# Performance work log

Hardware: AMD Instinct MI355X
Metric: run time of the kernel (lower is better)

Reference implementation:

```python
import jax, jax.numpy as jnp
import numpy as np

B, TT, C, H, T = 4, 4096, 1024, 16, 128
K = C // H  # head size (rk and v head sizes equal here)
HEAD_DIV = 8.0  # head_size_divisor
EPS = 1e-5  # GroupNorm eps
LAYER_ID, N_LAYER = 12, 24


def setup_inputs() -> dict:
    key = jax.random.key(0)
    ks = jax.random.split(key, 8)
    r01 = LAYER_ID / (N_LAYER - 1)
    r1a0 = 1.0 - LAYER_ID / N_LAYER
    ddd = (jnp.arange(C, dtype=jnp.float32) / C).reshape(1, 1, C)
    h = jnp.arange(H, dtype=jnp.float32)
    scale = 0.02
    return {
        "xq": jax.random.normal(ks[0], (B, TT, C), jnp.float32),
        "time_mix_k": ddd ** r1a0,
        "time_mix_v": ddd ** r1a0 + 0.3 * r01,
        "time_mix_r": ddd ** (0.5 * r1a0),
        "time_mix_g": ddd ** (0.5 * r1a0),
        "time_decay": -8.0 + 7.0 * (h / (H - 1)) ** (0.7 + 1.3 * r01),
        "time_faaaa": r01 * (1.0 - h / (H - 1)),
        "W_r": jax.random.normal(ks[1], (C, C), jnp.float32) * scale,
        "W_k": jax.random.normal(ks[2], (C, C), jnp.float32) * scale,
        "W_v": jax.random.normal(ks[3], (C, C), jnp.float32) * scale,
        "W_g": jax.random.normal(ks[4], (C, C), jnp.float32) * scale,
        "W_o": jax.random.normal(ks[5], (C, C), jnp.float32) * scale,
        "ln_w": jnp.ones((C,), jnp.float32),
        "ln_b": jnp.zeros((C,), jnp.float32),
    }


def reference(xq, time_mix_k, time_mix_v, time_mix_r, time_mix_g,
              time_decay, time_faaaa, W_r, W_k, W_v, W_g, W_o, ln_w, ln_b):
    x = xq
    B_, TT_, C_ = x.shape
    N = TT_ // T  # number of chunks
    # time shift: xx[:, t] = x[:, t-1], xx[:, 0] = 0
    xx = jnp.pad(x, ((0, 0), (1, 0), (0, 0)))[:, :-1]
    xr = x * time_mix_r + xx * (1 - time_mix_r)
    xk = x * time_mix_k + xx * (1 - time_mix_k)
    xv = x * time_mix_v + xx * (1 - time_mix_v)
    xg = x * time_mix_g + xx * (1 - time_mix_g)
    r = (xr @ W_r.T).reshape(B_, TT_, H, K).transpose(0, 2, 1, 3)  # (B,H,TT,K)
    k = (xk @ W_k.T).reshape(B_, TT_, H, K).transpose(0, 2, 1, 3)
    v = (xv @ W_v.T).reshape(B_, TT_, H, K).transpose(0, 2, 1, 3)
    g = jax.nn.silu(xg @ W_g.T)  # (B,TT,C)

    decay = jnp.exp(-jnp.exp(time_decay))  # (H,)
    u = time_faaaa  # (H,)
    ws = decay ** T  # per-chunk state decay (H,)
    i_idx = jnp.arange(T)
    wb = decay[:, None] ** i_idx                # (H,T): decay^i
    wk = decay[:, None] ** (T - 1 - i_idx)      # (H,T): decay^(T-1-j)
    diff = i_idx[:, None] - i_idx[None, :]      # i - j
    pw = decay[:, None, None] ** jnp.maximum(diff - 1, 0)
    # lower-triangular intra-chunk decay: decay^(i-j-1) for i>j, u on diag
    w_mat = jnp.where(diff > 0, pw, 0.0) + jnp.eye(T, dtype=x.dtype) * u[:, None, None]  # (H,T,T)

    # chunked layout: (N, B, H, T, K)
    rc = r.reshape(B_, H, N, T, K).transpose(2, 0, 1, 3, 4)
    kc = k.reshape(B_, H, N, T, K).transpose(2, 0, 1, 3, 4)
    vc = v.reshape(B_, H, N, T, K).transpose(2, 0, 1, 3, 4)
    s0 = jnp.zeros((B_, H, K, K), x.dtype)

    def step(s, chunk):
        rr, kk, vv = chunk
        att = jnp.einsum('bhik,bhjk->bhij', rr, kk) * w_mat
        out = att @ vv + jnp.einsum('bhik,bhkv->bhiv', rr, s) * wb[None, :, :, None]
        s_new = ws[None, :, None, None] * s + jnp.einsum(
            'bhjk,bhjv->bhkv', kk * wk[None, :, :, None], vv)
        return s_new, out

    _, xo = jax.lax.scan(step, s0, (rc, kc, vc))  # xo: (N,B,H,T,K)
    xo = xo.transpose(1, 0, 3, 2, 4).reshape(B_, TT_, H, K)

    # GroupNorm(H groups) over channels, applied to x / head_size_divisor
    y = xo / HEAD_DIV
    mu = y.mean(-1, keepdims=True)
    var = y.var(-1, keepdims=True)
    y = (y - mu) / jnp.sqrt(var + EPS)
    y = y * ln_w.reshape(H, K) + ln_b.reshape(H, K)
    y = y.reshape(B_, TT_, C_)
    return (y * g) @ W_o.T
```

## Files before the change

### kernel.cpp

```cpp
#include <hip/hip_runtime.h>
#include <hip/hip_bf16.h>
#include <stdint.h>

#define C_DIM 1024
#define H_DIM 16
#define K_DIM 64
#define T_CH 128
#define TT_DIM 4096
#define B_DIM 4
#define N_CH 32
#define M_ROWS 16384

typedef __attribute__((ext_vector_type(8))) __bf16 bf16x8;
typedef __attribute__((ext_vector_type(4))) float floatx4;

__device__ __forceinline__ float bf2f(ushort u) {
  union { uint32_t i; float f; } v; v.i = ((uint32_t)u) << 16; return v.f;
}
__device__ __forceinline__ ushort f2bf(float f) {
  union { float f; uint32_t i; } v; v.f = f;
  return (ushort)((v.i + 0x7fffu + ((v.i >> 16) & 1u)) >> 16);
}

#define GLOAD_LDS16(g, l)                                                     \
  __builtin_amdgcn_global_load_lds(                                           \
      (const __attribute__((address_space(1))) void*)(g),                     \
      (__attribute__((address_space(3))) void*)(l), 16, 0, 0)

__global__ __launch_bounds__(256) void mix_kernel(
    const float* __restrict__ x,
    const float* __restrict__ mk, const float* __restrict__ mv,
    const float* __restrict__ mr, const float* __restrict__ mg,
    ushort* __restrict__ xr, ushort* __restrict__ xk,
    ushort* __restrict__ xv, ushort* __restrict__ xg) {
  long idx = (long)blockIdx.x * 256 + threadIdx.x;
  long e = idx * 4;
  int c = (int)(e & (C_DIM - 1));
  long row = e >> 10;
  int t = (int)(row & (TT_DIM - 1));
  floatx4 xc = *(const floatx4*)(x + e);
  floatx4 xp = {0.f, 0.f, 0.f, 0.f};
  if (t != 0) xp = *(const floatx4*)(x + e - C_DIM);
  floatx4 d = xc - xp;
  floatx4 vk = *(const floatx4*)(mk + c);
  floatx4 vv = *(const floatx4*)(mv + c);
  floatx4 vr = *(const floatx4*)(mr + c);
  floatx4 vg = *(const floatx4*)(mg + c);
  floatx4 ok = xp + d * vk;
  floatx4 ov = xp + d * vv;
  floatx4 orr = xp + d * vr;
  floatx4 og = xp + d * vg;
  union { ushort u[4]; uint2 q; } pk;
#define ST(dst, val)                                                          \
  pk.u[0] = f2bf(val.x); pk.u[1] = f2bf(val.y);                               \
  pk.u[2] = f2bf(val.z); pk.u[3] = f2bf(val.w);                               \
  *(uint2*)((dst) + e) = pk.q;
  ST(xk, ok) ST(xv, ov) ST(xr, orr) ST(xg, og)
#undef ST
}

__global__ __launch_bounds__(256) void wconv_kernel(
    const float* __restrict__ w0, const float* __restrict__ w1,
    const float* __restrict__ w2, const float* __restrict__ w3,
    const float* __restrict__ w4, ushort* __restrict__ o) {
  long idx = (long)blockIdx.x * 256 + threadIdx.x;
  long e = idx * 4;
  int wi = (int)(e >> 20);
  long off = e & ((1L << 20) - 1);
  const float* src = wi == 0 ? w0 : wi == 1 ? w1 : wi == 2 ? w2 : wi == 3 ? w3 : w4;
  floatx4 vv = *(const floatx4*)(src + off);
  union { ushort u[4]; uint2 q; } pk;
  pk.u[0] = f2bf(vv.x); pk.u[1] = f2bf(vv.y);
  pk.u[2] = f2bf(vv.z); pk.u[3] = f2bf(vv.w);
  *(uint2*)(o + e) = pk.q;
}

#define BARX() __builtin_amdgcn_s_barrier()
#define SCHEDB() __builtin_amdgcn_sched_barrier(0)
#define VMW4() asm volatile("s_waitcnt vmcnt(4)" ::: "memory")
#define VMW0() asm volatile("s_waitcnt vmcnt(0)" ::: "memory")
#define LGKW() asm volatile("s_waitcnt lgkmcnt(0)" ::: "memory")

template <int EPI>
__global__ __launch_bounds__(512, 2) void gemm_bt(
    const ushort* __restrict__ A, const ushort* __restrict__ Bt,
    void* __restrict__ Cout) {
  __shared__ __align__(16) ushort smem[65536];
  const int tid = threadIdx.x;
  const int lane = tid & 63, w = tid >> 6;
  const int q = lane >> 4, l16 = lane & 15;
  const int wm = w >> 2, wn = w & 3;
  const int id = blockIdx.x;
  const int wg = (id & 7) * 32 + (id >> 3);
  const int bm = wg >> 2, bn = wg & 3;

  const int r8 = tid >> 3;
  const int c8 = ((tid & 7) ^ (r8 & 7)) * 8;
  const ushort* gA = A + (long)(bm * 256 + r8) * C_DIM + c8;
  const ushort* gB = Bt + (long)(bn * 256 + r8) * C_DIM + c8;

  const char* sB = (const char*)smem;
  const int arow = (wm * 128 + l16) * 128;
  const int brow = (wn * 64 + l16) * 128;
  const int swz = (l16 & 7) << 4;
  const int csv[2] = {(q << 4) ^ swz, ((4 + q) << 4) ^ swz};

  floatx4 acc[8][4] = {};
  bf16x8 af[4][2];
  bf16x8 bfv[4][2];

#define STAGE(ISA, sl, hh, tile)                                              \
  do {                                                                        \
    const ushort* g_ = (ISA ? gA : gB) + ((hh) * 131072 + (tile) * 64);       \
    ushort* l_ = smem + ((ISA ? 0 : 32768) + (sl) * 16384 + (hh) * 8192 +     \
                         w * 512);                                            \
    GLOAD_LDS16(g_, l_);                                                      \
    GLOAD_LDS16(g_ + 65536, l_ + 4096);                                       \
  } while (0)

#define READ_A(sl, qr)                                                        \
  do {                                                                        \
    _Pragma("unroll") for (int i_ = 0; i_ < 4; ++i_) {                        \
      af[i_][0] = *(const bf16x8*)(sB + (sl) * 32768 + arow + (qr) * 8192 +   \
                                   i_ * 2048 + csv[0]);                       \
      af[i_][1] = *(const bf16x8*)(sB + (sl) * 32768 + arow + (qr) * 8192 +   \
                                   i_ * 2048 + csv[1]);                       \
    }                                                                         \
  } while (0)

#define READ_B(sl, qc)                                                        \
  do {                                                                        \
    _Pragma("unroll") for (int j_ = 0; j_ < 2; ++j_) {                        \
      bfv[(qc) * 2 + j_][0] = *(const bf16x8*)(sB + 65536 + (sl) * 32768 +    \
                                               brow + (qc) * 4096 +           \
                                               j_ * 2048 + csv[0]);           \
      bfv[(qc) * 2 + j_][1] = *(const bf16x8*)(sB + 65536 + (sl) * 32768 +    \
                                               brow + (qc) * 4096 +           \
                                               j_ * 2048 + csv[1]);           \
    }                                                                         \
  } while (0)

#define MFMA_Q(qr, qc)                                                        \
  do {                                                                        \
    __builtin_amdgcn_s_setprio(1);                                            \
    _Pragma("unroll") for (int i_ = 0; i_ < 4; ++i_)                          \
        _Pragma("unroll") for (int j_ = 0; j_ < 2; ++j_) {                    \
      acc[(qr) * 4 + i_][(qc) * 2 + j_] =                                     \
          __builtin_amdgcn_mfma_f32_16x16x32_bf16(                            \
              af[i_][0], bfv[(qc) * 2 + j_][0],                               \
              acc[(qr) * 4 + i_][(qc) * 2 + j_], 0, 0, 0);                    \
      acc[(qr) * 4 + i_][(qc) * 2 + j_] =                                     \
          __builtin_amdgcn_mfma_f32_16x16x32_bf16(                            \
              af[i_][1], bfv[(qc) * 2 + j_][1],                               \
              acc[(qr) * 4 + i_][(qc) * 2 + j_], 0, 0, 0);                    \
    }                                                                         \
    __builtin_amdgcn_s_setprio(0);                                            \
  } while (0)

  STAGE(1, 0, 0, 0); STAGE(1, 0, 1, 0);
  STAGE(0, 0, 0, 0); STAGE(0, 0, 1, 0);
  STAGE(0, 1, 0, 1); STAGE(0, 1, 1, 1);
  VMW4();
  BARX();
  SCHEDB();
  READ_B(0, 0);

#pragma unroll 1
  for (int i = 0; i < 7; ++i) {
    const int t1 = 2 * i + 1, tn0 = 2 * i + 2, tn1 = 2 * i + 3;
    READ_A(0, 0); STAGE(1, 1, 0, t1);
    BARX(); SCHEDB(); READ_B(0, 1); MFMA_Q(0, 0); LGKW(); BARX();
    STAGE(1, 1, 1, t1);
    BARX(); SCHEDB(); MFMA_Q(0, 1); LGKW(); BARX();
    READ_A(0, 1); STAGE(0, 0, 0, tn0);
    BARX(); SCHEDB(); MFMA_Q(1, 0); LGKW(); BARX();
    STAGE(0, 0, 1, tn0); VMW4();
    BARX(); SCHEDB(); READ_B(1, 0); MFMA_Q(1, 1); LGKW(); BARX();
    READ_A(1, 0); STAGE(1, 0, 0, tn0);
    BARX(); SCHEDB(); READ_B(1, 1); MFMA_Q(0, 0); LGKW(); BARX();
    STAGE(1, 0, 1, tn0);
    BARX(); SCHEDB(); MFMA_Q(0, 1); LGKW(); BARX();
    READ_A(1, 1); STAGE(0, 1, 0, tn1);
    BARX(); SCHEDB(); MFMA_Q(1, 0); LGKW(); BARX();
    STAGE(0, 1, 1, tn1); VMW4();
    BARX(); SCHEDB(); READ_B(0, 0); MFMA_Q(1, 1); LGKW(); BARX();
  }
  READ_A(0, 0); STAGE(1, 1, 0, 15);
  BARX(); SCHEDB(); READ_B(0, 1); MFMA_Q(0, 0); LGKW(); BARX();
  STAGE(1, 1, 1, 15);
  BARX(); SCHEDB(); MFMA_Q(0, 1); LGKW(); BARX();
  READ_A(0, 1);
  BARX(); SCHEDB(); MFMA_Q(1, 0); LGKW(); BARX();
  VMW0();
  BARX(); SCHEDB(); READ_B(1, 0); MFMA_Q(1, 1); LGKW(); BARX();
  READ_A(1, 0);
  BARX(); SCHEDB(); READ_B(1, 1); MFMA_Q(0, 0); LGKW(); BARX();
  BARX(); SCHEDB(); MFMA_Q(0, 1); LGKW(); BARX();
  READ_A(1, 1);
  BARX(); SCHEDB(); MFMA_Q(1, 0); LGKW(); BARX();
  BARX(); MFMA_Q(1, 1);

  const int row0 = bm * 256 + wm * 128 + q * 4;
  const int col0 = bn * 256 + wn * 64 + l16;
#pragma unroll
  for (int fi = 0; fi < 8; ++fi)
#pragma unroll
    for (int fj = 0; fj < 4; ++fj)
#pragma unroll
      for (int rg = 0; rg < 4; ++rg) {
        long off = (long)(row0 + fi * 16 + rg) * C_DIM + col0 + fj * 16;
        float val = acc[fi][fj][rg];
        if (EPI == 1) val = val / (1.f + expf(-val));
        if (EPI == 2)
          ((float*)Cout)[off] = val;
        else
          ((ushort*)Cout)[off] = f2bf(val);
      }
#undef STAGE
#undef READ_A
#undef READ_B
#undef MFMA_Q
}

__global__ __launch_bounds__(256) void chunk_state(
    const ushort* __restrict__ kB, const ushort* __restrict__ vB,
    const float* __restrict__ td, ushort* __restrict__ Zc) {
  __shared__ __align__(16) ushort vt_s[64 * 136];
  __shared__ __align__(16) ushort kwt_s[64 * 136];
  int blk = blockIdx.x;
  int bh = blk >> 5, n = blk & 31;
  int b = bh >> 4, h = bh & 15;
  int tid = threadIdx.x;
  int lane = tid & 63, w = tid >> 6;
  int q = lane >> 4, l16 = lane & 15;
  float etd = expf(td[h]);
  long cbase = ((long)b * TT_DIM + n * T_CH) * C_DIM + h * K_DIM;

#pragma unroll
  for (int it = 0; it < 4; it++) {
    int chunk = it * 256 + tid;
    int row = chunk >> 3;
    int cc = (chunk & 7) * 8;
    long ga = cbase + (long)row * C_DIM + cc;
    uint4 kv4 = *(const uint4*)(kB + ga);
    uint4 vv4 = *(const uint4*)(vB + ga);
    float wkj = expf(-(float)(T_CH - 1 - row) * etd);
    const ushort* kp = (const ushort*)&kv4;
    const ushort* vp = (const ushort*)&vv4;
    int cb2 = row >> 3;
#pragma unroll
    for (int e2 = 0; e2 < 8; e2++) {
      int vr = cc + e2;
      int ph = vr * 136 + ((cb2 ^ ((vr >> 3) & 7)) << 3) + (row & 7);
      kwt_s[ph] = f2bf(bf2f(kp[e2]) * wkj);
      vt_s[ph] = vp[e2];
    }
  }
  __syncthreads();

  floatx4 accZ[4] = {};
#pragma unroll
  for (int js = 0; js < 128; js += 32) {
    int cb = q + (js >> 3);
    int vrA = w * 16 + l16;
    bf16x8 av = *(const bf16x8*)&vt_s[vrA * 136 + ((cb ^ ((vrA >> 3) & 7)) << 3)];
    bf16x8 bk3[4];
#pragma unroll
    for (int kt = 0; kt < 4; kt++) {
      int vrB = kt * 16 + l16;
      bk3[kt] = *(const bf16x8*)&kwt_s[vrB * 136 + ((cb ^ ((vrB >> 3) & 7)) << 3)];
    }
#pragma unroll
    for (int kt = 0; kt < 4; kt++)
      accZ[kt] = __builtin_amdgcn_mfma_f32_16x16x32_bf16(av, bk3[kt], accZ[kt], 0, 0, 0);
  }
  long zbase = (long)blk * 4096;
#pragma unroll
  for (int kt = 0; kt < 4; kt++)
#pragma unroll
    for (int rg = 0; rg < 4; rg++)
      Zc[zbase + (w * 16 + q * 4 + rg) * 64 + kt * 16 + l16] = f2bf(accZ[kt][rg]);
}

__global__ __launch_bounds__(256) void state_scan(
    const ushort* __restrict__ Zc, const float* __restrict__ td,
    ushort* __restrict__ Sb) {
  long tg = (long)blockIdx.x * 256 + threadIdx.x;
  int bh = (int)(tg >> 12);
  int e = (int)(tg & 4095);
  int h = bh & 15;
  float wsf = expf(-128.f * expf(td[h]));
  float s = 0.f;
  long base = (long)bh * N_CH * 4096 + e;
#pragma unroll
  for (int n = 0; n < N_CH; n++) {
    Sb[base + n * 4096] = f2bf(s);
    s = wsf * s + bf2f(Zc[base + n * 4096]);
  }
}

__global__ __launch_bounds__(512, 4) void chunk_out(
    const ushort* __restrict__ rB, const ushort* __restrict__ kB,
    const ushort* __restrict__ vB, const ushort* __restrict__ gBuf,
    const ushort* __restrict__ Sb,
    const float* __restrict__ td, const float* __restrict__ tf,
    const float* __restrict__ lnw, const float* __restrict__ lnb,
    ushort* __restrict__ gy) {
  __shared__ __align__(16) ushort rr_s[128 * 72];
  __shared__ __align__(16) ushort un_s[128 * 136];
  __shared__ __align__(16) ushort vt_s[64 * 136];
  __shared__ __align__(16) ushort z_s[64 * 72];
  __shared__ float pw_s[128];

  int blk = blockIdx.x;
  int bh = blk >> 5, n = blk & 31;
  int b = bh >> 4, h = bh & 15;
  int tid = threadIdx.x;
  int lane = tid & 63, w = tid >> 6;
  int q = lane >> 4, l16 = lane & 15;

  float etd = expf(td[h]);
  float u = tf[h];
  long cbase = ((long)b * TT_DIM + n * T_CH) * C_DIM + h * K_DIM;

  if (tid < 128) pw_s[tid] = expf(-(float)tid * etd);

#pragma unroll
  for (int it = 0; it < 2; it++) {
    int chunk = it * 512 + tid;
    int row = chunk >> 3;
    int cc = (chunk & 7) * 8;
    long ga = cbase + (long)row * C_DIM + cc;
    *(uint4*)&rr_s[row * 72 + cc] = *(const uint4*)(rB + ga);
    *(uint4*)&un_s[row * 136 + cc] = *(const uint4*)(kB + ga);
    uint4 vv4 = *(const uint4*)(vB + ga);
    const ushort* vp = (const ushort*)&vv4;
    int cb2 = row >> 3;
#pragma unroll
    for (int e2 = 0; e2 < 8; e2++) {
      int vr = cc + e2;
      vt_s[vr * 136 + ((cb2 ^ ((vr >> 3) & 7)) << 3) + (row & 7)] = vp[e2];
    }
  }
  {
    long sbase = (long)blk * 4096;
    int v = tid >> 3, c0 = (tid & 7) * 8;
    *(uint4*)&z_s[v * 72 + c0] = *(const uint4*)(Sb + sbase + v * 64 + c0);
  }
  __syncthreads();

  int ar0 = (w >> 1) * 32, ac0 = (w & 1) * 64;
  floatx4 accA[2][4] = {};
#pragma unroll
  for (int ks = 0; ks < 64; ks += 32) {
    bf16x8 af[2], bk2[4];
#pragma unroll
    for (int i = 0; i < 2; i++)
      af[i] = *(const bf16x8*)&rr_s[(ar0 + i * 16 + l16) * 72 + q * 8 + ks];
#pragma unroll
    for (int j = 0; j < 4; j++)
      bk2[j] = *(const bf16x8*)&un_s[(ac0 + j * 16 + l16) * 136 + q * 8 + ks];
#pragma unroll
    for (int mi = 0; mi < 2; mi++)
#pragma unroll
      for (int nj = 0; nj < 4; nj++)
        accA[mi][nj] = __builtin_amdgcn_mfma_f32_16x16x32_bf16(
            af[mi], bk2[nj], accA[mi][nj], 0, 0, 0);
  }

  int i0 = w * 16;
  floatx4 accB[4] = {};
#pragma unroll
  for (int ks = 0; ks < 64; ks += 32) {
    bf16x8 af2 = *(const bf16x8*)&rr_s[(i0 + l16) * 72 + q * 8 + ks];
    bf16x8 bz[4];
#pragma unroll
    for (int vt2 = 0; vt2 < 4; vt2++)
      bz[vt2] = *(const bf16x8*)&z_s[(vt2 * 16 + l16) * 72 + q * 8 + ks];
#pragma unroll
    for (int vt2 = 0; vt2 < 4; vt2++)
      accB[vt2] = __builtin_amdgcn_mfma_f32_16x16x32_bf16(
          af2, bz[vt2], accB[vt2], 0, 0, 0);
  }
  __syncthreads();

#pragma unroll
  for (int mi = 0; mi < 2; mi++)
#pragma unroll
    for (int nj = 0; nj < 4; nj++)
#pragma unroll
      for (int rg = 0; rg < 4; rg++) {
        int i = ar0 + mi * 16 + q * 4 + rg;
        int j = ac0 + nj * 16 + l16;
        float wv = 0.f;
        if (i > j) wv = pw_s[i - j - 1];
        else if (i == j) wv = u;
        un_s[i * 136 + j] = f2bf(accA[mi][nj][rg] * wv);
      }
  __syncthreads();

  floatx4 accO[4] = {};
#pragma unroll
  for (int js = 0; js < 128; js += 32) {
    bf16x8 af3 = *(const bf16x8*)&un_s[(i0 + l16) * 136 + q * 8 + js];
    int cb = q + (js >> 3);
    bf16x8 bv[4];
#pragma unroll
    for (int vt2 = 0; vt2 < 4; vt2++) {
      int vr = vt2 * 16 + l16;
      bv[vt2] = *(const bf16x8*)&vt_s[vr * 136 + ((cb ^ ((vr >> 3) & 7)) << 3)];
    }
#pragma unroll
    for (int vt2 = 0; vt2 < 4; vt2++)
      accO[vt2] = __builtin_amdgcn_mfma_f32_16x16x32_bf16(
          af3, bv[vt2], accO[vt2], 0, 0, 0);
  }

#pragma unroll
  for (int rg = 0; rg < 4; rg++) {
    int i = i0 + q * 4 + rg;
    float wbi = pw_s[i];
    float vals[4];
    float s1 = 0.f, s2 = 0.f;
#pragma unroll
    for (int vt2 = 0; vt2 < 4; vt2++) {
      float val = accO[vt2][rg] + wbi * accB[vt2][rg];
      vals[vt2] = val; s1 += val; s2 += val * val;
    }
#pragma unroll
    for (int mm = 1; mm < 16; mm <<= 1) {
      s1 += __shfl_xor(s1, mm, 64);
      s2 += __shfl_xor(s2, mm, 64);
    }
    float mu = s1 * (1.f / 64.f);
    float va = s2 * (1.f / 64.f) - mu * mu;
    float rinv = rsqrtf(va + 64.f * 1e-5f);
    long rowg = (long)b * TT_DIM + n * T_CH + i;
#pragma unroll
    for (int vt2 = 0; vt2 < 4; vt2++) {
      int c = h * K_DIM + vt2 * 16 + l16;
      float y = (vals[vt2] - mu) * rinv * lnw[c] + lnb[c];
      float gf = bf2f(gBuf[rowg * C_DIM + c]);
      gy[rowg * C_DIM + c] = f2bf(y * gf);
    }
  }
}

extern "C" void kernel_launch(void* const* d_in, const int* in_sizes, int n_in,
                              void* d_out, int out_size, void* d_ws,
                              size_t ws_size, hipStream_t stream) {
  const float* xq  = (const float*)d_in[0];
  const float* tmk = (const float*)d_in[1];
  const float* tmv = (const float*)d_in[2];
  const float* tmr = (const float*)d_in[3];
  const float* tmg = (const float*)d_in[4];
  const float* td  = (const float*)d_in[5];
  const float* tf  = (const float*)d_in[6];
  const float* Wr  = (const float*)d_in[7];
  const float* Wk  = (const float*)d_in[8];
  const float* Wv  = (const float*)d_in[9];
  const float* Wg  = (const float*)d_in[10];
  const float* Wo  = (const float*)d_in[11];
  const float* lnw = (const float*)d_in[12];
  const float* lnb = (const float*)d_in[13];

  char* ws = (char*)d_ws;
  const size_t BUF = (size_t)M_ROWS * C_DIM * 2;
  ushort* b0 = (ushort*)(ws + 0 * BUF);
  ushort* b1 = (ushort*)(ws + 1 * BUF);
  ushort* b2 = (ushort*)(ws + 2 * BUF);
  ushort* b3 = (ushort*)(ws + 3 * BUF);
  ushort* wcv = (ushort*)(ws + 4 * BUF);
  const ushort* wr_b = wcv;
  const ushort* wk_b = wcv + (1 << 20);
  const ushort* wv_b = wcv + 2 * (1 << 20);
  const ushort* wg_b = wcv + 3 * (1 << 20);
  const ushort* wo_b = wcv + 4 * (1 << 20);
  ushort* Zc = (ushort*)(ws + 4 * BUF + 5 * (2 << 20));
  ushort* Sb = Zc + (size_t)64 * N_CH * 4096;
  ushort* rbuf = (ushort*)d_out;

  mix_kernel<<<16384, 256, 0, stream>>>(xq, tmk, tmv, tmr, tmg, b0, b1, b2, b3);
  wconv_kernel<<<5120, 256, 0, stream>>>(Wr, Wk, Wv, Wg, Wo, wcv);

  gemm_bt<0><<<256, 512, 0, stream>>>(b0, wr_b, rbuf);
  gemm_bt<0><<<256, 512, 0, stream>>>(b1, wk_b, b0);
  gemm_bt<0><<<256, 512, 0, stream>>>(b2, wv_b, b1);
  gemm_bt<1><<<256, 512, 0, stream>>>(b3, wg_b, b2);

  chunk_state<<<2048, 256, 0, stream>>>(b0, b1, td, Zc);
  state_scan<<<1024, 256, 0, stream>>>(Zc, td, Sb);
  chunk_out<<<2048, 512, 0, stream>>>(rbuf, b0, b1, b2, Sb, td, tf, lnw, lnb, b3);

  gemm_bt<2><<<256, 512, 0, stream>>>(b3, wo_b, (float*)d_out);
}
```

Before: 407.3 us.

## Pair projection GEMMs into shared launches and widen elementwise kernels to 8 elements

Combines the four input projection GEMMs into two launches of 512 workgroups each, so every launch fills the GPU with two independent GEMMs rather than 256 workgroups at a time. Buffers are reassigned so r and k land in the two halves of the fp32 output buffer, which serves as scratch. The mix and weight-conversion kernels now handle 8 elements per thread with 16-byte stores, halving their grid sizes. The aim is less launch overhead and better CU occupancy during the projections. This relies on the output buffer being large enough to hold two bf16 activation tensors before the final GEMM overwrites it.

```diff
diff --git a/kernel.cpp b/kernel.cpp
--- a/kernel.cpp
+++ b/kernel.cpp
@@ -34,28 +34,34 @@
     ushort* __restrict__ xr, ushort* __restrict__ xk,
     ushort* __restrict__ xv, ushort* __restrict__ xg) {
   long idx = (long)blockIdx.x * 256 + threadIdx.x;
-  long e = idx * 4;
+  long e = idx * 8;
   int c = (int)(e & (C_DIM - 1));
   long row = e >> 10;
   int t = (int)(row & (TT_DIM - 1));
-  floatx4 xc = *(const floatx4*)(x + e);
-  floatx4 xp = {0.f, 0.f, 0.f, 0.f};
-  if (t != 0) xp = *(const floatx4*)(x + e - C_DIM);
-  floatx4 d = xc - xp;
-  floatx4 vk = *(const floatx4*)(mk + c);
-  floatx4 vv = *(const floatx4*)(mv + c);
-  floatx4 vr = *(const floatx4*)(mr + c);
-  floatx4 vg = *(const floatx4*)(mg + c);
-  floatx4 ok = xp + d * vk;
-  floatx4 ov = xp + d * vv;
-  floatx4 orr = xp + d * vr;
-  floatx4 og = xp + d * vg;
-  union { ushort u[4]; uint2 q; } pk;
-#define ST(dst, val)                                                          \
-  pk.u[0] = f2bf(val.x); pk.u[1] = f2bf(val.y);                               \
-  pk.u[2] = f2bf(val.z); pk.u[3] = f2bf(val.w);                               \
-  *(uint2*)((dst) + e) = pk.q;
-  ST(xk, ok) ST(xv, ov) ST(xr, orr) ST(xg, og)
+  floatx4 xc0 = *(const floatx4*)(x + e);
+  floatx4 xc1 = *(const floatx4*)(x + e + 4);
+  floatx4 xp0 = {0.f, 0.f, 0.f, 0.f};
+  floatx4 xp1 = {0.f, 0.f, 0.f, 0.f};
+  if (t != 0) {
+    xp0 = *(const floatx4*)(x + e - C_DIM);
+    xp1 = *(const floatx4*)(x + e - C_DIM + 4);
+  }
+  floatx4 d0 = xc0 - xp0;
+  floatx4 d1 = xc1 - xp1;
+  union { ushort u[8]; uint4 q; } pk;
+#define ST(dst, mptr)                                                         \
+  {                                                                           \
+    floatx4 m0 = *(const floatx4*)((mptr) + c);                               \
+    floatx4 m1 = *(const floatx4*)((mptr) + c + 4);                           \
+    floatx4 o0 = xp0 + d0 * m0;                                               \
+    floatx4 o1 = xp1 + d1 * m1;                                               \
+    pk.u[0] = f2bf(o0.x); pk.u[1] = f2bf(o0.y);                               \
+    pk.u[2] = f2bf(o0.z); pk.u[3] = f2bf(o0.w);                               \
+    pk.u[4] = f2bf(o1.x); pk.u[5] = f2bf(o1.y);                               \
+    pk.u[6] = f2bf(o1.z); pk.u[7] = f2bf(o1.w);                               \
+    *(uint4*)((dst) + e) = pk.q;                                              \
+  }
+  ST(xk, mk) ST(xv, mv) ST(xr, mr) ST(xg, mg)
 #undef ST
 }
 
@@ -64,15 +70,18 @@
     const float* __restrict__ w2, const float* __restrict__ w3,
     const float* __restrict__ w4, ushort* __restrict__ o) {
   long idx = (long)blockIdx.x * 256 + threadIdx.x;
-  long e = idx * 4;
+  long e = idx * 8;
   int wi = (int)(e >> 20);
   long off = e & ((1L << 20) - 1);
   const float* src = wi == 0 ? w0 : wi == 1 ? w1 : wi == 2 ? w2 : wi == 3 ? w3 : w4;
-  floatx4 vv = *(const floatx4*)(src + off);
-  union { ushort u[4]; uint2 q; } pk;
-  pk.u[0] = f2bf(vv.x); pk.u[1] = f2bf(vv.y);
-  pk.u[2] = f2bf(vv.z); pk.u[3] = f2bf(vv.w);
-  *(uint2*)(o + e) = pk.q;
+  floatx4 v0 = *(const floatx4*)(src + off);
+  floatx4 v1 = *(const floatx4*)(src + off + 4);
+  union { ushort u[8]; uint4 q; } pk;
+  pk.u[0] = f2bf(v0.x); pk.u[1] = f2bf(v0.y);
+  pk.u[2] = f2bf(v0.z); pk.u[3] = f2bf(v0.w);
+  pk.u[4] = f2bf(v1.x); pk.u[5] = f2bf(v1.y);
+  pk.u[6] = f2bf(v1.z); pk.u[7] = f2bf(v1.w);
+  *(uint4*)(o + e) = pk.q;
 }
 
 #define BARX() __builtin_amdgcn_s_barrier()
@@ -82,17 +91,13 @@
 #define LGKW() asm volatile("s_waitcnt lgkmcnt(0)" ::: "memory")
 
 template <int EPI>
-__global__ __launch_bounds__(512, 2) void gemm_bt(
+__device__ __forceinline__ void gemm_body(
     const ushort* __restrict__ A, const ushort* __restrict__ Bt,
-    void* __restrict__ Cout) {
-  __shared__ __align__(16) ushort smem[65536];
+    void* __restrict__ Cout, ushort* smem, int bm, int bn) {
   const int tid = threadIdx.x;
   const int lane = tid & 63, w = tid >> 6;
   const int q = lane >> 4, l16 = lane & 15;
   const int wm = w >> 2, wn = w & 3;
-  const int id = blockIdx.x;
-  const int wg = (id & 7) * 32 + (id >> 3);
-  const int bm = wg >> 2, bn = wg & 3;
 
   const int r8 = tid >> 3;
   const int c8 = ((tid & 7) ^ (r8 & 7)) * 8;
@@ -222,6 +227,33 @@
 #undef MFMA_Q
 }
 
+template <int EPI>
+__global__ __launch_bounds__(512, 2) void gemm_bt(
+    const ushort* __restrict__ A, const ushort* __restrict__ Bt,
+    void* __restrict__ Cout) {
+  __shared__ __align__(16) ushort smem[65536];
+  const int id = blockIdx.x;
+  const int wg = (id & 7) * 32 + (id >> 3);
+  gemm_body<EPI>(A, Bt, Cout, smem, wg >> 2, wg & 3);
+}
+
+template <int EPI1>
+__global__ __launch_bounds__(512, 2) void gemm_pair(
+    const ushort* __restrict__ A0, const ushort* __restrict__ B0,
+    void* __restrict__ C0,
+    const ushort* __restrict__ A1, const ushort* __restrict__ B1,
+    void* __restrict__ C1) {
+  __shared__ __align__(16) ushort smem[65536];
+  const int id = blockIdx.x;
+  const int wgg = (id & 7) * 64 + (id >> 3);
+  const int inner = wgg & 255;
+  const int bm = inner >> 2, bn = inner & 3;
+  if (wgg < 256)
+    gemm_body<0>(A0, B0, C0, smem, bm, bn);
+  else
+    gemm_body<EPI1>(A1, B1, C1, smem, bm, bn);
+}
+
 __global__ __launch_bounds__(256) void chunk_state(
     const ushort* __restrict__ kB, const ushort* __restrict__ vB,
     const float* __restrict__ td, ushort* __restrict__ Zc) {
@@ -478,19 +510,18 @@
   const ushort* wo_b = wcv + 4 * (1 << 20);
   ushort* Zc = (ushort*)(ws + 4 * BUF + 5 * (2 << 20));
   ushort* Sb = Zc + (size_t)64 * N_CH * 4096;
-  ushort* rbuf = (ushort*)d_out;
-
-  mix_kernel<<<16384, 256, 0, stream>>>(xq, tmk, tmv, tmr, tmg, b0, b1, b2, b3);
-  wconv_kernel<<<5120, 256, 0, stream>>>(Wr, Wk, Wv, Wg, Wo, wcv);
-
-  gemm_bt<0><<<256, 512, 0, stream>>>(b0, wr_b, rbuf);
-  gemm_bt<0><<<256, 512, 0, stream>>>(b1, wk_b, b0);
-  gemm_bt<0><<<256, 512, 0, stream>>>(b2, wv_b, b1);
-  gemm_bt<1><<<256, 512, 0, stream>>>(b3, wg_b, b2);
-
-  chunk_state<<<2048, 256, 0, stream>>>(b0, b1, td, Zc);
+  ushort* dL = (ushort*)d_out;
+  ushort* dH = dL + (size_t)M_ROWS * C_DIM;
+
+  mix_kernel<<<8192, 256, 0, stream>>>(xq, tmk, tmv, tmr, tmg, b0, b1, b2, b3);
+  wconv_kernel<<<2560, 256, 0, stream>>>(Wr, Wk, Wv, Wg, Wo, wcv);
+
+  gemm_pair<0><<<512, 512, 0, stream>>>(b0, wr_b, dL, b1, wk_b, dH);
+  gemm_pair<1><<<512, 512, 0, stream>>>(b2, wv_b, b0, b3, wg_b, b1);
+
+  chunk_state<<<2048, 256, 0, stream>>>(dH, b0, td, Zc);
   state_scan<<<1024, 256, 0, stream>>>(Zc, td, Sb);
-  chunk_out<<<2048, 512, 0, stream>>>(rbuf, b0, b1, b2, Sb, td, tf, lnw, lnb, b3);
-
-  gemm_bt<2><<<256, 512, 0, stream>>>(b3, wo_b, (float*)d_out);
-}
+  chunk_out<<<2048, 512, 0, stream>>>(dL, dH, b0, b1, Sb, td, tf, lnw, lnb, b2);
+
+  gemm_bt<2><<<256, 512, 0, stream>>>(b2, wo_b, (float*)d_out);
+}
```

After: 412.8 us. Within noise of the previous version (+1.3%).
